# Optimization experiments

Measured on AMD Instinct MI355X. Metric: run time of the kernel, lower is better.

The kernel has to match this reference:

```python
import jax, jax.numpy as jnp
import numpy as np

C32 = 768      # channels at stride 32 (convnextv2)
E = 4          # num_experts


def setup_inputs() -> dict:
    key = jax.random.key(0)
    ks = jax.random.split(key, 12)
    s = 0.02
    inp = {
        "s4":  jax.random.normal(ks[0], (8, 96, 256, 256), jnp.float32),
        "s8":  jax.random.normal(ks[1], (8, 192, 128, 128), jnp.float32),
        "s16": jax.random.normal(ks[2], (8, 384, 64, 64), jnp.float32),
        "s32": jax.random.normal(ks[3], (8, C32, 32, 32), jnp.float32),
        # 2-layer gate: C -> C -> E
        "gate_w1": jax.random.normal(ks[4], (C32, C32), jnp.float32) * s,
        "gate_b1": jnp.zeros((C32,), jnp.float32),
        "gate_w2": jax.random.normal(ks[5], (C32, E), jnp.float32) * s,
        "gate_b2": jnp.zeros((E,), jnp.float32),
        # E stacked ProtoExpert MLPs: C -> C -> C
        "exp_w1": jax.random.normal(ks[6], (E, C32, C32), jnp.float32) * s,
        "exp_b1": jnp.zeros((E, C32), jnp.float32),
        "exp_w2": jax.random.normal(ks[7], (E, C32, C32), jnp.float32) * s,
        "exp_b2": jnp.zeros((E, C32), jnp.float32),
    }
    return inp


def _vision_moe(x_bchw, gate_w1, gate_b1, gate_w2, gate_b2, exp_w1, exp_b1, exp_w2, exp_b2):
    B, C, H, W = x_bchw.shape
    x = x_bchw.transpose(0, 2, 3, 1).reshape(-1, C)            # [N, C] tokens
    # 2-layer gate -> softmax -> top-1 routing
    logits = jax.nn.gelu(x @ gate_w1 + gate_b1) @ gate_w2 + gate_b2  # [N, E]
    probs = jax.nn.softmax(logits, axis=-1)
    top_idx = jnp.argmax(probs, axis=-1)                        # [N]
    gate_val = jnp.take_along_axis(probs, top_idx[:, None], axis=-1)  # [N, 1]
    # dense all-expert compute, then select routed expert (jit-friendly)
    h = jax.nn.gelu(jnp.einsum('nc,ecd->ned', x, exp_w1) + exp_b1)    # [N, E, C]
    y_all = jnp.einsum('ned,edf->nef', h, exp_w2) + exp_b2            # [N, E, C]
    onehot = jax.nn.one_hot(top_idx, probs.shape[-1], dtype=x.dtype)  # [N, E]
    y = jnp.einsum('nef,ne->nf', y_all, onehot) * gate_val            # [N, C]
    return y.reshape(B, H, W, C).transpose(0, 3, 1, 2)


def reference(s4, s8, s16, s32, gate_w1, gate_b1, gate_w2, gate_b2, exp_w1, exp_b1, exp_w2, exp_b2):
    out32 = _vision_moe(s32, gate_w1, gate_b1, gate_w2, gate_b2,
                        exp_w1, exp_b1, exp_w2, exp_b2) + s32
    return (s4, s8, s16, out32)
```

## Files before the change

### kernel.cpp

```cpp
#include <hip/hip_runtime.h>
#include <cstddef>

#define CCH 768
#define CHUNK 262144u

#define OFF_YT    0u
#define OFF_HH    25165824u
#define OFF_W2T   37748736u
#define OFF_IDX   42467328u
#define OFF_PERM  42500096u
#define OFF_CNT   42532864u
#define OFF_CUR   42532880u
#define OFF_GVAL  42532896u
#define OFF_PART  42565664u
#define TAILBYTES 44564480u
#define OFF_XL    44564480u
#define OFF_GWH   57147392u
#define OFF_GWL   58327040u
#define OFF_XH    59506688u
#define OFF_W1T   72089600u
#define S8DST     201326592u
#define S16DST    301989888u
#define OUTDST    352321536u

typedef __attribute__((ext_vector_type(8))) short short8v;
typedef __attribute__((ext_vector_type(4))) float f32x4;

__device__ __forceinline__ void gl16(const void* g, void* l) {
    __builtin_amdgcn_global_load_lds(
        (const __attribute__((address_space(1))) void*)g,
        (__attribute__((address_space(3))) void*)l, 16, 0, 0);
}

__device__ __forceinline__ void copy_chunk_raw(const char* src, char* dst) {
    const uint4* s = (const uint4*)src;
    uint4* d = (uint4*)dst;
    int t = threadIdx.x;
#pragma unroll 8
    for (int it = 0; it < 64; ++it) d[it * 256 + t] = s[it * 256 + t];
}

__device__ __forceinline__ float gelu_tanh(float x) {
    float u = 0.7978845608028654f * (x + 0.044715f * x * x * x);
    float e = __expf(2.0f * u);
    float t = 1.0f - 2.0f / (e + 1.0f);
    return 0.5f * x * (1.0f + t);
}

__device__ __forceinline__ short f2b(float f) {
    unsigned u = __float_as_uint(f);
    unsigned r = (u + 0x7FFFu + ((u >> 16) & 1u)) >> 16;
    return (short)r;
}

__global__ __launch_bounds__(256) void k_prep(const float* __restrict__ s32,
                                              const float* __restrict__ gw1,
                                              short* __restrict__ Xh,
                                              short* __restrict__ Xl,
                                              short* __restrict__ GWh,
                                              short* __restrict__ GWl,
                                              int* __restrict__ az) {
    int z = blockIdx.z;
    int tx = threadIdx.x, ty = threadIdx.y;
    if (z == 0 && blockIdx.x == 0 && blockIdx.y == 0 && ty == 0 && tx < 8)
        az[tx] = 0;
    __shared__ float tile[32][33];
    if (z < 8) {
        int c0 = blockIdx.y * 32, hw0 = blockIdx.x * 32;
        const float* s = s32 + (size_t)z * CCH * 1024;
#pragma unroll
        for (int i = 0; i < 4; ++i)
            tile[ty + 8 * i][tx] = s[(size_t)(c0 + ty + 8 * i) * 1024 + hw0 + tx];
        __syncthreads();
#pragma unroll
        for (int i = 0; i < 4; ++i) {
            int r = ty + 8 * i;
            int n = z * 1024 + hw0 + r;
            float v = tile[tx][r];
            short h = f2b(v);
            float vh = __uint_as_float(((unsigned)(unsigned short)h) << 16);
            Xh[(size_t)n * CCH + c0 + tx] = h;
            Xl[(size_t)n * CCH + c0 + tx] = f2b(v - vh);
        }
    } else {
        if (blockIdx.x >= 24) return;
        int ci0 = blockIdx.x * 32, co0 = blockIdx.y * 32;
#pragma unroll
        for (int i = 0; i < 4; ++i)
            tile[ty + 8 * i][tx] = gw1[(size_t)(ci0 + ty + 8 * i) * CCH + co0 + tx];
        __syncthreads();
#pragma unroll
        for (int i = 0; i < 4; ++i) {
            int co = co0 + ty + 8 * i;
            float v = tile[tx][ty + 8 * i];
            short h = f2b(v);
            GWh[(size_t)co * CCH + ci0 + tx] = h;
            float vh = __uint_as_float(((unsigned)(unsigned short)h) << 16);
            GWl[(size_t)co * CCH + ci0 + tx] = f2b(v - vh);
        }
    }
}

template <int MODE>
__global__ __launch_bounds__(256) void k_mfma(const short* __restrict__ Ahp,
                                              const short* __restrict__ Alp,
                                              const short* __restrict__ Bhp,
                                              const short* __restrict__ Blp,
                                              const float* __restrict__ bias,
                                              const float* __restrict__ gw2,
                                              const int* __restrict__ perm,
                                              const int* __restrict__ counts,
                                              const float* __restrict__ gval,
                                              float* __restrict__ Yt,
                                              short* __restrict__ Hout,
                                              float* __restrict__ partial,
                                              const float* __restrict__ ew1,
                                              const float* __restrict__ ew2,
                                              short* __restrict__ W1T,
                                              short* __restrict__ W2T,
                                              const char* __restrict__ csrc1,
                                              const char* __restrict__ csrc2,
                                              char* __restrict__ bb,
                                              int ngemm) {
    __shared__ __align__(16) short lds[32768];
    int bid = blockIdx.x;
    int t = threadIdx.x;
    if (bid >= ngemm) {
        int i = bid - ngemm;
        if (MODE == 0) {
            if (i < 475) {
                size_t c = (size_t)(293 + i) * CHUNK;
                copy_chunk_raw(csrc1 + c, bb + c);
            } else if (i < 859) {
                size_t o = (size_t)(i - 475) * CHUNK;
                copy_chunk_raw(csrc2 + o, bb + S8DST + o);
            } else {
                int j = i - 859;
                int mat = j / 576, q = j % 576;
                int ci0 = (q % 24) * 32, co0 = (q / 24) * 32;
                const float* src = (mat < 4 ? ew1 : ew2) + (size_t)(mat & 3) * CCH * CCH;
                short* dst = (mat < 4 ? W1T : W2T) + (size_t)(mat & 3) * CCH * CCH;
                float* tile = (float*)lds;
                int tx = t & 31, ty = t >> 5;
#pragma unroll
                for (int i4 = 0; i4 < 4; ++i4)
                    tile[(ty + 8 * i4) * 33 + tx] =
                        src[(size_t)(ci0 + ty + 8 * i4) * CCH + co0 + tx];
                __syncthreads();
#pragma unroll
                for (int i4 = 0; i4 < 4; ++i4) {
                    int co = co0 + ty + 8 * i4;
                    dst[(size_t)co * CCH + ci0 + tx] = f2b(tile[tx * 33 + ty + 8 * i4]);
                }
            }
        } else if (MODE == 1) {
            if (i < 57) {
                size_t c = (size_t)(170 + i) * CHUNK;
                copy_chunk_raw(csrc1 + c, bb + c);
            } else {
                size_t o = (size_t)(i - 57) * CHUNK;
                copy_chunk_raw(csrc2 + o, bb + S16DST + o);
            }
        } else {
            if (i < 66) {
                size_t c = (size_t)(227 + i) * CHUNK;
                copy_chunk_raw(csrc1 + c, bb + c);
            } else {
                size_t o = (size_t)(96 + i - 66) * CHUNK;
                copy_chunk_raw(csrc2 + (size_t)(i - 66) * CHUNK, bb + S16DST + o - (size_t)96 * CHUNK + (size_t)96 * CHUNK);
            }
        }
        return;
    }

    int cbk = bid % 6;
    int mt = bid / 6;
    int c0 = cbk * 128;
    int e = 0, ts = mt, cnt = 1 << 30, ofs = 0, mrow0 = 0;
    if (MODE == 0) {
        mrow0 = mt * 128;
    } else {
        e = mt >> 6;
        ts = mt & 63;
        int n0 = counts[0], n1 = counts[1], n2 = counts[2], n3 = counts[3];
        cnt = (e == 0) ? n0 : (e == 1) ? n1 : (e == 2) ? n2 : n3;
        if (ts * 128 >= cnt) return;
        ofs = (e > 0 ? n0 : 0) + (e > 1 ? n1 : 0) + (e > 2 ? n2 : 0);
    }

    int lane = t & 63, w = t >> 6;
    int wr = w >> 1, wc = w & 1;
    int lrow = lane & 15, lk8 = lane >> 4;

    const short* aS[4];
    const short* bS[4];
    const short* alS[2];
    const short* blS[2];
    int dA[4];

    if (MODE == 0) {
#pragma unroll
        for (int i = 0; i < 2; ++i) {
            int c = 2 * w + i;
            int row = c * 16 + lrow;
            int koff = lk8 * 8;
            aS[i]  = Ahp + (size_t)(mrow0 + row) * CCH + koff;
            alS[i] = Alp + (size_t)(mrow0 + row) * CCH + koff;
            bS[i]  = Bhp + (size_t)(c0 + row) * CCH + koff;
            blS[i] = Blp + (size_t)(c0 + row) * CCH + koff;
            dA[i] = c * 512;
        }
    } else {
        size_t eoff = (size_t)e * CCH * CCH;
#pragma unroll
        for (int i = 0; i < 4; ++i) {
            int c = 4 * w + i;
            int g = c >> 1, ph = c & 1;
            int row = g * 16 + lrow;
            int koff = ph * 32 + lk8 * 8;
            int pl = ts * 128 + row;
            int pc = pl < cnt ? pl : cnt - 1;
            int tokrow = (MODE == 1) ? perm[ofs + pc] : (ofs + pc);
            aS[i] = Ahp + (size_t)tokrow * CCH + koff;
            bS[i] = Bhp + eoff + (size_t)(c0 + row) * CCH + koff;
            dA[i] = c * 512;
        }
    }

    f32x4 acc[4][4] = {};

    if (MODE == 0) {
        auto stage = [&](int b, int k0) {
            short* L = lds + b * 16384;
#pragma unroll
            for (int i = 0; i < 2; ++i) {
                gl16(aS[i] + k0, L + dA[i]);
                gl16(bS[i] + k0, L + 4096 + dA[i]);
                gl16(alS[i] + k0, L + 8192 + dA[i]);
                gl16(blS[i] + k0, L + 12288 + dA[i]);
            }
        };
        stage(0, 0);
        __syncthreads();
        for (int tt = 0; tt < 24; ++tt) {
            int cur = tt & 1;
            if (tt < 23) stage(cur ^ 1, (tt + 1) * 32);
            const short* L = lds + cur * 16384;
            short8v af[4], bf[4], xf[4];
#pragma unroll
            for (int m = 0; m < 4; ++m)
                af[m] = *(const short8v*)(L + ((wr * 4 + m) * 64 + lane) * 8);
#pragma unroll
            for (int n = 0; n < 4; ++n)
                bf[n] = *(const short8v*)(L + 4096 + ((wc * 4 + n) * 64 + lane) * 8);
#pragma unroll
            for (int m = 0; m < 4; ++m)
#pragma unroll
                for (int n = 0; n < 4; ++n)
                    acc[m][n] = __builtin_amdgcn_mfma_f32_16x16x32_bf16(af[m], bf[n], acc[m][n], 0, 0, 0);
#pragma unroll
            for (int n = 0; n < 4; ++n)
                xf[n] = *(const short8v*)(L + 12288 + ((wc * 4 + n) * 64 + lane) * 8);
#pragma unroll
            for (int m = 0; m < 4; ++m)
#pragma unroll
                for (int n = 0; n < 4; ++n)
                    acc[m][n] = __builtin_amdgcn_mfma_f32_16x16x32_bf16(af[m], xf[n], acc[m][n], 0, 0, 0);
#pragma unroll
            for (int m = 0; m < 4; ++m)
                xf[m] = *(const short8v*)(L + 8192 + ((wr * 4 + m) * 64 + lane) * 8);
#pragma unroll
            for (int m = 0; m < 4; ++m)
#pragma unroll
                for (int n = 0; n < 4; ++n)
                    acc[m][n] = __builtin_amdgcn_mfma_f32_16x16x32_bf16(xf[m], bf[n], acc[m][n], 0, 0, 0);
            __syncthreads();
        }
    } else {
        auto stage = [&](int b, int k0) {
            short* L = lds + b * 16384;
#pragma unroll
            for (int i = 0; i < 4; ++i) {
                gl16(aS[i] + k0, L + dA[i]);
                gl16(bS[i] + k0, L + 8192 + dA[i]);
            }
        };
        stage(0, 0);
        __syncthreads();
        for (int tt = 0; tt < 12; ++tt) {
            int cur = tt & 1;
            if (tt < 11) stage(cur ^ 1, (tt + 1) * 64);
            const short* L = lds + cur * 16384;
#pragma unroll
            for (int kk = 0; kk < 2; ++kk) {
                short8v af[4], bf[4];
#pragma unroll
                for (int m = 0; m < 4; ++m)
                    af[m] = *(const short8v*)(L + (((wr * 4 + m) * 2 + kk) * 64 + lane) * 8);
#pragma unroll
                for (int n = 0; n < 4; ++n)
                    bf[n] = *(const short8v*)(L + 8192 + (((wc * 4 + n) * 2 + kk) * 64 + lane) * 8);
#pragma unroll
                for (int m = 0; m < 4; ++m)
#pragma unroll
                    for (int n = 0; n < 4; ++n)
                        acc[m][n] = __builtin_amdgcn_mfma_f32_16x16x32_bf16(af[m], bf[n], acc[m][n], 0, 0, 0);
            }
            __syncthreads();
        }
    }

    int cl = lane & 15, rh = (lane >> 4) * 4;
    if (MODE == 0) {
        int cb2 = cbk * 2 + wc;
        float bv[4];
        float4 w2v[4];
#pragma unroll
        for (int n_ = 0; n_ < 4; ++n_) {
            int col = c0 + wc * 64 + n_ * 16 + cl;
            bv[n_] = bias[col];
            w2v[n_] = *(const float4*)(gw2 + col * 4);
        }
#pragma unroll
        for (int m = 0; m < 4; ++m) {
#pragma unroll
            for (int ri = 0; ri < 4; ++ri) {
                float s0 = 0.f, s1 = 0.f, s2 = 0.f, s3 = 0.f;
#pragma unroll
                for (int n_ = 0; n_ < 4; ++n_) {
                    float g = gelu_tanh(acc[m][n_][ri] + bv[n_]);
                    s0 = fmaf(g, w2v[n_].x, s0);
                    s1 = fmaf(g, w2v[n_].y, s1);
                    s2 = fmaf(g, w2v[n_].z, s2);
                    s3 = fmaf(g, w2v[n_].w, s3);
                }
#pragma unroll
                for (int off = 1; off < 16; off <<= 1) {
                    s0 += __shfl_xor(s0, off);
                    s1 += __shfl_xor(s1, off);
                    s2 += __shfl_xor(s2, off);
                    s3 += __shfl_xor(s3, off);
                }
                if (cl == 0) {
                    int row = mrow0 + wr * 64 + m * 16 + rh + ri;
                    float4 pv;
                    pv.x = s0; pv.y = s1; pv.z = s2; pv.w = s3;
                    *(float4*)(partial + (size_t)(cb2 * 8192 + row) * 4) = pv;
                }
            }
        }
    } else {
#pragma unroll
        for (int n = 0; n < 4; ++n) {
            int col = c0 + wc * 64 + n * 16 + cl;
            float bv = bias[e * CCH + col];
#pragma unroll
            for (int m = 0; m < 4; ++m) {
#pragma unroll
                for (int ri = 0; ri < 4; ++ri) {
                    int p = ts * 128 + wr * 64 + m * 16 + rh + ri;
                    if (p < cnt) {
                        float v = acc[m][n][ri] + bv;
                        if (MODE == 1) {
                            Hout[(size_t)(ofs + p) * CCH + col] = f2b(gelu_tanh(v));
                        } else {
                            int nn = perm[ofs + p];
                            Yt[(size_t)nn * CCH + col] = v * gval[nn];
                        }
                    }
                }
            }
        }
    }
}

__global__ __launch_bounds__(256) void k_route(const float* __restrict__ partial,
                                               const float* __restrict__ b2,
                                               int* __restrict__ idx,
                                               float* __restrict__ gval,
                                               int* __restrict__ counts) {
    int n = blockIdx.x * 256 + threadIdx.x;
    float l0 = b2[0], l1 = b2[1], l2 = b2[2], l3 = b2[3];
#pragma unroll
    for (int p = 0; p < 12; ++p) {
        float4 v = *(const float4*)(partial + ((size_t)p * 8192 + n) * 4);
        l0 += v.x; l1 += v.y; l2 += v.z; l3 += v.w;
    }
    int e = 0;
    float m = l0;
    if (l1 > m) { m = l1; e = 1; }
    if (l2 > m) { m = l2; e = 2; }
    if (l3 > m) { m = l3; e = 3; }
    float s = __expf(l0 - m) + __expf(l1 - m) + __expf(l2 - m) + __expf(l3 - m);
    idx[n] = e;
    gval[n] = 1.0f / s;
    atomicAdd(counts + e, 1);
}

__global__ __launch_bounds__(256) void k_scatter(const int* __restrict__ idx,
                                                 const int* __restrict__ counts,
                                                 int* __restrict__ cursors,
                                                 int* __restrict__ perm) {
    int n = blockIdx.x * 256 + threadIdx.x;
    int e = idx[n];
    int run = 0;
#pragma unroll
    for (int ee = 0; ee < 4; ++ee) {
        int c = counts[ee];
        if (e == ee) {
            int pos = run + atomicAdd(cursors + ee, 1);
            perm[pos] = n;
        }
        run += c;
    }
}

__global__ __launch_bounds__(256) void k_untr(const float* __restrict__ Yt,
                                              const float* __restrict__ s32,
                                              float* __restrict__ out32) {
    __shared__ float tile[32][33];
    int b = blockIdx.z;
    int c0 = blockIdx.y * 32, hw0 = blockIdx.x * 32;
    int tx = threadIdx.x, ty = threadIdx.y;
#pragma unroll
    for (int i = 0; i < 4; ++i) {
        int hwl = ty + 8 * i;
        tile[hwl][tx] = Yt[(size_t)(b * 1024 + hw0 + hwl) * CCH + c0 + tx];
    }
    __syncthreads();
    const float* sp = s32 + (size_t)b * CCH * 1024;
    float* op = out32 + (size_t)b * CCH * 1024;
#pragma unroll
    for (int i = 0; i < 4; ++i) {
        size_t a = (size_t)(c0 + ty + 8 * i) * 1024 + hw0 + tx;
        op[a] = tile[tx][ty + 8 * i] + sp[a];
    }
}

extern "C" void kernel_launch(void* const* d_in, const int* in_sizes, int n_in,
                              void* d_out, int out_size, void* d_ws, size_t ws_size,
                              hipStream_t stream) {
    const float* s4  = (const float*)d_in[0];
    const float* s8  = (const float*)d_in[1];
    const float* s16 = (const float*)d_in[2];
    const float* s32 = (const float*)d_in[3];
    const float* gw1 = (const float*)d_in[4];
    const float* gb1 = (const float*)d_in[5];
    const float* gw2 = (const float*)d_in[6];
    const float* gb2 = (const float*)d_in[7];
    const float* ew1 = (const float*)d_in[8];
    const float* eb1 = (const float*)d_in[9];
    const float* ew2 = (const float*)d_in[10];
    const float* eb2 = (const float*)d_in[11];

    char* bb = (char*)d_out;
    float* Yt      = (float*)(bb + OFF_YT);
    short* Hh      = (short*)(bb + OFF_HH);
    short* W2T     = (short*)(bb + OFF_W2T);
    int*   idx     = (int*)(bb + OFF_IDX);
    int*   perm    = (int*)(bb + OFF_PERM);
    int*   counts  = (int*)(bb + OFF_CNT);
    int*   cursors = (int*)(bb + OFF_CUR);
    float* gval    = (float*)(bb + OFF_GVAL);
    float* partial = (float*)(bb + OFF_PART);
    short* Xl      = (short*)(bb + OFF_XL);
    short* GWh     = (short*)(bb + OFF_GWH);
    short* GWl     = (short*)(bb + OFF_GWL);
    short* Xh      = (short*)(bb + OFF_XH);
    short* W1T     = (short*)(bb + OFF_W1T);
    float* out32   = (float*)(bb + OUTDST);

    k_prep<<<dim3(32, 24, 9), dim3(32, 8), 0, stream>>>(s32, gw1, Xh, Xl, GWh, GWl, counts);
    k_mfma<0><<<384 + 859 + 4608, 256, 0, stream>>>(Xh, Xl, GWh, GWl, gb1, gw2,
                                                    perm, counts, gval, Yt, Hh,
                                                    partial, ew1, ew2, W1T, W2T,
                                                    (const char*)s4, (const char*)s8,
                                                    bb, 384);
    k_route<<<32, 256, 0, stream>>>(partial, gb2, idx, gval, counts);
    k_scatter<<<32, 256, 0, stream>>>(idx, counts, cursors, perm);
    k_mfma<1><<<1536 + 153, 256, 0, stream>>>(Xh, Xl, W1T, GWl, eb1, gw2,
                                              perm, counts, gval, Yt, Hh,
                                              partial, ew1, ew2, W1T, W2T,
                                              (const char*)s4, (const char*)s16,
                                              bb, 1536);
    k_mfma<2><<<1536 + 162, 256, 0, stream>>>(Hh, Xl, W2T, GWl, eb2, gw2,
                                              perm, counts, gval, Yt, Hh,
                                              partial, ew1, ew2, W1T, W2T,
                                              (const char*)s4, (const char*)(s16 + (size_t)96 * CHUNK / 4),
                                              bb, 1536);
    k_untr<<<dim3(32, 24, 8), dim3(32, 8), 0, stream>>>(Yt, s32, out32);
    hipMemcpyAsync(bb, s4, (size_t)TAILBYTES, hipMemcpyDeviceToDevice, stream);
}
```

Baseline: 371.5 us.

## Move scratch to workspace and spread passthrough copies across all kernels

Scratch buffers move from the output buffer into the workspace when it is large enough. This lets every passthrough chunk be copied by extra blocks inside the GEMM and untranspose kernels instead of a trailing serialized device memcpy. Copy counts are rebalanced per stage, and the untranspose kernel is flattened to a 1D grid so it can carry copy blocks too. If the workspace is too small, it falls back to the old layout with a tail memcpy.

```diff
diff --git a/kernel.cpp b/kernel.cpp
--- a/kernel.cpp
+++ b/kernel.cpp
@@ -4,24 +4,17 @@
 #define CCH 768
 #define CHUNK 262144u
 
-#define OFF_YT    0u
-#define OFF_HH    25165824u
-#define OFF_W2T   37748736u
-#define OFF_IDX   42467328u
-#define OFF_PERM  42500096u
-#define OFF_CNT   42532864u
-#define OFF_CUR   42532880u
-#define OFF_GVAL  42532896u
-#define OFF_PART  42565664u
-#define TAILBYTES 44564480u
-#define OFF_XL    44564480u
-#define OFF_GWH   57147392u
-#define OFF_GWL   58327040u
-#define OFF_XH    59506688u
-#define OFF_W1T   72089600u
-#define S8DST     201326592u
-#define S16DST    301989888u
-#define OUTDST    352321536u
+#define OFF_XH    0u
+#define OFF_XL    12582912u
+#define OFF_GWH   25165824u
+#define OFF_GWL   26345472u
+#define OFF_W1T   27525120u
+#define OFF_W2T   32243712u
+#define OFF_HH    36962304u
+#define OFF_YT    49545216u
+#define OFF_PART  74711040u
+#define OFF_AUX   76283904u
+#define SCRATCH_NEED 76349440u
 
 typedef __attribute__((ext_vector_type(8))) short short8v;
 typedef __attribute__((ext_vector_type(4))) float f32x4;
@@ -32,9 +25,13 @@
         (__attribute__((address_space(3))) void*)l, 16, 0, 0);
 }
 
-__device__ __forceinline__ void copy_chunk_raw(const char* src, char* dst) {
+__device__ __forceinline__ void copy_chunk(int g, const char* s4b, const char* s8b,
+                                           const char* s16b, char* bb) {
+    const char* src = (g < 768) ? s4b + (size_t)g * CHUNK
+                    : (g < 1152) ? s8b + (size_t)(g - 768) * CHUNK
+                                 : s16b + (size_t)(g - 1152) * CHUNK;
     const uint4* s = (const uint4*)src;
-    uint4* d = (uint4*)dst;
+    uint4* d = (uint4*)(bb + (size_t)g * CHUNK);
     int t = threadIdx.x;
 #pragma unroll 8
     for (int it = 0; it < 64; ++it) d[it * 256 + t] = s[it * 256 + t];
@@ -118,56 +115,35 @@
                                               const float* __restrict__ ew2,
                                               short* __restrict__ W1T,
                                               short* __restrict__ W2T,
-                                              const char* __restrict__ csrc1,
-                                              const char* __restrict__ csrc2,
+                                              const char* __restrict__ s4b,
+                                              const char* __restrict__ s8b,
+                                              const char* __restrict__ s16b,
                                               char* __restrict__ bb,
-                                              int ngemm) {
+                                              int ngemm, int ncopy, int cbase) {
     __shared__ __align__(16) short lds[32768];
     int bid = blockIdx.x;
     int t = threadIdx.x;
     if (bid >= ngemm) {
         int i = bid - ngemm;
-        if (MODE == 0) {
-            if (i < 475) {
-                size_t c = (size_t)(293 + i) * CHUNK;
-                copy_chunk_raw(csrc1 + c, bb + c);
-            } else if (i < 859) {
-                size_t o = (size_t)(i - 475) * CHUNK;
-                copy_chunk_raw(csrc2 + o, bb + S8DST + o);
-            } else {
-                int j = i - 859;
-                int mat = j / 576, q = j % 576;
-                int ci0 = (q % 24) * 32, co0 = (q / 24) * 32;
-                const float* src = (mat < 4 ? ew1 : ew2) + (size_t)(mat & 3) * CCH * CCH;
-                short* dst = (mat < 4 ? W1T : W2T) + (size_t)(mat & 3) * CCH * CCH;
-                float* tile = (float*)lds;
-                int tx = t & 31, ty = t >> 5;
-#pragma unroll
-                for (int i4 = 0; i4 < 4; ++i4)
-                    tile[(ty + 8 * i4) * 33 + tx] =
-                        src[(size_t)(ci0 + ty + 8 * i4) * CCH + co0 + tx];
-                __syncthreads();
-#pragma unroll
-                for (int i4 = 0; i4 < 4; ++i4) {
-                    int co = co0 + ty + 8 * i4;
-                    dst[(size_t)co * CCH + ci0 + tx] = f2b(tile[tx * 33 + ty + 8 * i4]);
-                }
-            }
-        } else if (MODE == 1) {
-            if (i < 57) {
-                size_t c = (size_t)(170 + i) * CHUNK;
-                copy_chunk_raw(csrc1 + c, bb + c);
-            } else {
-                size_t o = (size_t)(i - 57) * CHUNK;
-                copy_chunk_raw(csrc2 + o, bb + S16DST + o);
-            }
-        } else {
-            if (i < 66) {
-                size_t c = (size_t)(227 + i) * CHUNK;
-                copy_chunk_raw(csrc1 + c, bb + c);
-            } else {
-                size_t o = (size_t)(96 + i - 66) * CHUNK;
-                copy_chunk_raw(csrc2 + (size_t)(i - 66) * CHUNK, bb + S16DST + o - (size_t)96 * CHUNK + (size_t)96 * CHUNK);
+        if (i < ncopy) {
+            copy_chunk(cbase + i, s4b, s8b, s16b, bb);
+        } else if (MODE == 0) {
+            int j = i - ncopy;
+            int mat = j / 576, q = j % 576;
+            int ci0 = (q % 24) * 32, co0 = (q / 24) * 32;
+            const float* src = (mat < 4 ? ew1 : ew2) + (size_t)(mat & 3) * CCH * CCH;
+            short* dst = (mat < 4 ? W1T : W2T) + (size_t)(mat & 3) * CCH * CCH;
+            float* tile = (float*)lds;
+            int tx = t & 31, ty = t >> 5;
+#pragma unroll
+            for (int i4 = 0; i4 < 4; ++i4)
+                tile[(ty + 8 * i4) * 33 + tx] =
+                    src[(size_t)(ci0 + ty + 8 * i4) * CCH + co0 + tx];
+            __syncthreads();
+#pragma unroll
+            for (int i4 = 0; i4 < 4; ++i4) {
+                int co = co0 + ty + 8 * i4;
+                dst[(size_t)co * CCH + ci0 + tx] = f2b(tile[tx * 33 + ty + 8 * i4]);
             }
         }
         return;
@@ -417,11 +393,24 @@
 
 __global__ __launch_bounds__(256) void k_untr(const float* __restrict__ Yt,
                                               const float* __restrict__ s32,
-                                              float* __restrict__ out32) {
+                                              float* __restrict__ out32,
+                                              const char* __restrict__ s4b,
+                                              const char* __restrict__ s8b,
+                                              const char* __restrict__ s16b,
+                                              char* __restrict__ bb,
+                                              int ncopy, int cbase) {
+    int bid = blockIdx.x;
+    if (bid >= 6144) {
+        int i = bid - 6144;
+        if (i < ncopy) copy_chunk(cbase + i, s4b, s8b, s16b, bb);
+        return;
+    }
     __shared__ float tile[32][33];
-    int b = blockIdx.z;
-    int c0 = blockIdx.y * 32, hw0 = blockIdx.x * 32;
-    int tx = threadIdx.x, ty = threadIdx.y;
+    int hw0 = (bid & 31) * 32;
+    int c0 = ((bid >> 5) % 24) * 32;
+    int b = bid / 768;
+    int t = threadIdx.x;
+    int tx = t & 31, ty = t >> 5;
 #pragma unroll
     for (int i = 0; i < 4; ++i) {
         int hwl = ty + 8 * i;
@@ -453,41 +442,55 @@
     const float* ew2 = (const float*)d_in[10];
     const float* eb2 = (const float*)d_in[11];
 
+    bool WS = ws_size >= (size_t)SCRATCH_NEED;
     char* bb = (char*)d_out;
-    float* Yt      = (float*)(bb + OFF_YT);
-    short* Hh      = (short*)(bb + OFF_HH);
-    short* W2T     = (short*)(bb + OFF_W2T);
-    int*   idx     = (int*)(bb + OFF_IDX);
-    int*   perm    = (int*)(bb + OFF_PERM);
-    int*   counts  = (int*)(bb + OFF_CNT);
-    int*   cursors = (int*)(bb + OFF_CUR);
-    float* gval    = (float*)(bb + OFF_GVAL);
-    float* partial = (float*)(bb + OFF_PART);
-    short* Xl      = (short*)(bb + OFF_XL);
-    short* GWh     = (short*)(bb + OFF_GWH);
-    short* GWl     = (short*)(bb + OFF_GWL);
-    short* Xh      = (short*)(bb + OFF_XH);
-    short* W1T     = (short*)(bb + OFF_W1T);
-    float* out32   = (float*)(bb + OUTDST);
-
-    k_prep<<<dim3(32, 24, 9), dim3(32, 8), 0, stream>>>(s32, gw1, Xh, Xl, GWh, GWl, counts);
-    k_mfma<0><<<384 + 859 + 4608, 256, 0, stream>>>(Xh, Xl, GWh, GWl, gb1, gw2,
-                                                    perm, counts, gval, Yt, Hh,
-                                                    partial, ew1, ew2, W1T, W2T,
-                                                    (const char*)s4, (const char*)s8,
-                                                    bb, 384);
+    char* sb = WS ? (char*)d_ws : bb;
+
+    short* Xh      = (short*)(sb + OFF_XH);
+    short* Xl      = (short*)(sb + OFF_XL);
+    short* GWh     = (short*)(sb + OFF_GWH);
+    short* GWl     = (short*)(sb + OFF_GWL);
+    short* W1T     = (short*)(sb + OFF_W1T);
+    short* W2T     = (short*)(sb + OFF_W2T);
+    short* Hh      = (short*)(sb + OFF_HH);
+    float* Yt      = (float*)(sb + OFF_YT);
+    float* partial = (float*)(sb + OFF_PART);
+    int*   iaux    = (int*)(sb + OFF_AUX);
+    int*   idx     = iaux;
+    int*   perm    = iaux + 8192;
+    int*   counts  = iaux + 16384;
+    int*   cursors = iaux + 16388;
+    float* gval    = (float*)(iaux + 16392);
+    float* out32   = (float*)(bb + (size_t)1344 * CHUNK);
+
+    int cb = WS ? 0 : 292;
+    int n0 = 560, n1 = 300, n2 = 300;
+    int rem = 1344 - cb - n0 - n1 - n2;
+    int n3 = rem > 0 ? rem : 0;
+    if (rem < 0) n2 += rem;
+    int b0 = cb, b1 = b0 + n0, b2o = b1 + n1, b3 = b2o + n2;
+
+    k_prep<<<dim3(32, 24, 9), dim3(32, 8), 0, stream>>>(s32, gw1, Xh, Xl, GWh, GWl, iaux + 16384);
+    k_mfma<0><<<384 + n0 + 4608, 256, 0, stream>>>(Xh, Xl, GWh, GWl, gb1, gw2,
+                                                   perm, counts, gval, Yt, Hh,
+                                                   partial, ew1, ew2, W1T, W2T,
+                                                   (const char*)s4, (const char*)s8,
+                                                   (const char*)s16, bb, 384, n0, b0);
     k_route<<<32, 256, 0, stream>>>(partial, gb2, idx, gval, counts);
     k_scatter<<<32, 256, 0, stream>>>(idx, counts, cursors, perm);
-    k_mfma<1><<<1536 + 153, 256, 0, stream>>>(Xh, Xl, W1T, GWl, eb1, gw2,
-                                              perm, counts, gval, Yt, Hh,
-                                              partial, ew1, ew2, W1T, W2T,
-                                              (const char*)s4, (const char*)s16,
-                                              bb, 1536);
-    k_mfma<2><<<1536 + 162, 256, 0, stream>>>(Hh, Xl, W2T, GWl, eb2, gw2,
-                                              perm, counts, gval, Yt, Hh,
-                                              partial, ew1, ew2, W1T, W2T,
-                                              (const char*)s4, (const char*)(s16 + (size_t)96 * CHUNK / 4),
-                                              bb, 1536);
-    k_untr<<<dim3(32, 24, 8), dim3(32, 8), 0, stream>>>(Yt, s32, out32);
-    hipMemcpyAsync(bb, s4, (size_t)TAILBYTES, hipMemcpyDeviceToDevice, stream);
-}
+    k_mfma<1><<<1536 + n1, 256, 0, stream>>>(Xh, Xl, W1T, GWl, eb1, gw2,
+                                             perm, counts, gval, Yt, Hh,
+                                             partial, ew1, ew2, W1T, W2T,
+                                             (const char*)s4, (const char*)s8,
+                                             (const char*)s16, bb, 1536, n1, b1);
+    k_mfma<2><<<1536 + n2, 256, 0, stream>>>(Hh, Xl, W2T, GWl, eb2, gw2,
+                                             perm, counts, gval, Yt, Hh,
+                                             partial, ew1, ew2, W1T, W2T,
+                                             (const char*)s4, (const char*)s8,
+                                             (const char*)s16, bb, 1536, n2, b2o);
+    k_untr<<<6144 + n3, 256, 0, stream>>>(Yt, s32, out32,
+                                          (const char*)s4, (const char*)s8,
+                                          (const char*)s16, bb, n3, b3);
+    if (!WS)
+        hipMemcpyAsync(bb, s4, (size_t)cb * CHUNK, hipMemcpyDeviceToDevice, stream);
+}
```

Result: slower. 469.0 us (+26.2%).
